# Kernel tuning notes

Hardware: AMD Instinct MI355X
Metric: run time of the kernel (lower is better)

Reference implementation:

```python
import jax, jax.numpy as jnp
import numpy as np

N = 50000      # nodes
E = 800000     # edges (before self loops)
IN_DIM = 128
HID = 16
HEADS = 8
OUT_DIM = 40
NEG_SLOPE = 0.2


def setup_inputs() -> dict:
    key = jax.random.key(0)
    ks = jax.random.split(key, 10)
    x = jax.random.normal(ks[0], (N, IN_DIM), jnp.float32)
    edge_index = jax.random.randint(ks[1], (2, E), 0, N, dtype=jnp.int32)
    # layer 1: GATConv(IN_DIM, HID, heads=HEADS, concat=True)
    W1 = jax.random.normal(ks[2], (IN_DIM, HEADS * HID), jnp.float32) / np.sqrt(IN_DIM).astype(np.float32)
    att_src1 = jax.random.normal(ks[3], (HEADS, HID), jnp.float32) * 0.1
    att_dst1 = jax.random.normal(ks[4], (HEADS, HID), jnp.float32) * 0.1
    bias1 = jnp.zeros((HEADS * HID,), jnp.float32)
    # layer 2: GATConv(HEADS*HID, OUT_DIM, heads=1, concat=False)
    W2 = jax.random.normal(ks[5], (HEADS * HID, OUT_DIM), jnp.float32) / np.sqrt(HEADS * HID).astype(np.float32)
    att_src2 = jax.random.normal(ks[6], (1, OUT_DIM), jnp.float32) * 0.1
    att_dst2 = jax.random.normal(ks[7], (1, OUT_DIM), jnp.float32) * 0.1
    bias2 = jnp.zeros((OUT_DIM,), jnp.float32)
    return {"x": x, "W1": W1, "att_src1": att_src1, "att_dst1": att_dst1, "bias1": bias1,
            "W2": W2, "att_src2": att_src2, "att_dst2": att_dst2, "bias2": bias2,
            "edge_index": edge_index}


def gat_conv(x, src, dst, W, att_src, att_dst, bias, heads, dim, concat, num_nodes):
    # h: [N, H, D]
    h = (x @ W).reshape(num_nodes, heads, dim)
    a_src = jnp.sum(h * att_src, axis=-1)  # [N, H]
    a_dst = jnp.sum(h * att_dst, axis=-1)  # [N, H]
    e = a_src[src] + a_dst[dst]            # [E', H]
    e = jnp.where(e > 0, e, NEG_SLOPE * e)  # leaky_relu
    # segment softmax over edges sharing the same target node
    m = jax.ops.segment_max(e, dst, num_segments=num_nodes)  # [N, H]
    e = jnp.exp(e - m[dst])
    s = jax.ops.segment_sum(e, dst, num_segments=num_nodes)  # [N, H]
    alpha = e / (s[dst] + 1e-16)            # [E', H]
    msg = h[src] * alpha[:, :, None]        # [E', H, D]
    out = jax.ops.segment_sum(msg, dst, num_segments=num_nodes)  # [N, H, D]
    if concat:
        out = out.reshape(num_nodes, heads * dim)
    else:
        out = out.mean(axis=1)
    return out + bias


def reference(x, W1, att_src1, att_dst1, bias1, W2, att_src2, att_dst2, bias2, edge_index):
    # add self loops (PyG GATConv default)
    loop = jnp.arange(N, dtype=edge_index.dtype)
    src = jnp.concatenate([edge_index[0], loop])
    dst = jnp.concatenate([edge_index[1], loop])
    # eval mode: dropout (p=0.6) is identity
    h = gat_conv(x, src, dst, W1, att_src1, att_dst1, bias1, HEADS, HID, True, N)
    h = jax.nn.elu(h)
    out = gat_conv(h, src, dst, W2, att_src2, att_dst2, bias2, 1, OUT_DIM, False, N)
    return jax.nn.log_softmax(out, axis=1)
```

## Files before the change

### kernel.cpp

```cpp
#include <hip/hip_runtime.h>
#include <math.h>

#define IN_DIM 128
#define HEADS 8
#define HID 16
#define OUT_DIM 40
#define NEG 0.2f
#define NSLICE 8

typedef short bf16x8 __attribute__((ext_vector_type(8)));
typedef float f32x4 __attribute__((ext_vector_type(4)));

__device__ __forceinline__ unsigned short f32_to_bf16_rne(float v) {
  unsigned u = __float_as_uint(v);
  return (unsigned short)((u + 0x7FFFu + ((u >> 16) & 1u)) >> 16);
}


__global__ void hist_k(const int* __restrict__ ei, int E0, int N, int snode,
                       int* __restrict__ deg) {
  int b = blockIdx.x;
  int slice = b & (NSLICE - 1);
  int e = (b >> 3) * 256 + threadIdx.x;
  int EP = E0 + N;
  if (e >= EP) return;
  int d = (e < E0) ? ei[E0 + e] : (e - E0);
  if (d / snode == slice) atomicAdd(&deg[d], 1);
}

__global__ __launch_bounds__(1024) void scanA_k(const int* __restrict__ deg, int* __restrict__ rp,
                                                int* __restrict__ bsum, int n) {
  __shared__ int wsum[16];
  int tid = threadIdx.x;
  int i = blockIdx.x * 1024 + tid;
  int lane = tid & 63, w = tid >> 6;
  int v = (i < n) ? deg[i] : 0;
  int x = v;
  #pragma unroll
  for (int off = 1; off < 64; off <<= 1) {
    int y = __shfl_up(x, off);
    if (lane >= off) x += y;
  }
  if (lane == 63) wsum[w] = x;
  __syncthreads();
  if (tid < 16) {
    int s = wsum[tid];
    #pragma unroll
    for (int off = 1; off < 16; off <<= 1) {
      int y = __shfl_up(s, off);
      if (tid >= off) s += y;
    }
    wsum[tid] = s;
  }
  __syncthreads();
  int woff = (w == 0) ? 0 : wsum[w - 1];
  if (i < n) rp[i] = woff + x - v;
  if (tid == 0) bsum[blockIdx.x] = wsum[15];
}

__global__ __launch_bounds__(1024) void scanB_k(int* __restrict__ bsum, int nb,
                                                int* __restrict__ rp, int n) {
  __shared__ int wsum[16];
  int tid = threadIdx.x;
  int lane = tid & 63, w = tid >> 6;
  int v = (tid < nb) ? bsum[tid] : 0;
  int x = v;
  #pragma unroll
  for (int off = 1; off < 64; off <<= 1) {
    int y = __shfl_up(x, off);
    if (lane >= off) x += y;
  }
  if (lane == 63) wsum[w] = x;
  __syncthreads();
  if (tid < 16) {
    int s = wsum[tid];
    #pragma unroll
    for (int off = 1; off < 16; off <<= 1) {
      int y = __shfl_up(s, off);
      if (tid >= off) s += y;
    }
    wsum[tid] = s;
  }
  __syncthreads();
  int woff = (w == 0) ? 0 : wsum[w - 1];
  if (tid < nb) bsum[tid] = woff + x - v;
  if (tid == 0) rp[n] = wsum[15];
}

__global__ __launch_bounds__(1024) void scanC_k(int* __restrict__ rp, const int* __restrict__ bsum,
                                                int* __restrict__ cnt, int n) {
  int i = blockIdx.x * 1024 + threadIdx.x;
  if (i < n) {
    int v = rp[i] + bsum[blockIdx.x];
    rp[i] = v;
    cnt[i] = v;
  }
}

__global__ void scatter_k(const int* __restrict__ ei, int E0, int N, int snode,
                          int* __restrict__ cnt, int* __restrict__ csr_src) {
  int b = blockIdx.x;
  int slice = b & (NSLICE - 1);
  int e = (b >> 3) * 256 + threadIdx.x;
  int EP = E0 + N;
  if (e >= EP) return;
  int d = (e < E0) ? ei[E0 + e] : (e - E0);
  if (d / snode != slice) return;
  int s = (e < E0) ? ei[e] : d;
  int pos = atomicAdd(&cnt[d], 1);
  csr_src[pos] = s;
}

__global__ void prep_k(const float* __restrict__ W1, const float* __restrict__ as1,
                       const float* __restrict__ ad1, const float* __restrict__ W2,
                       const float* __restrict__ as2, const float* __restrict__ ad2,
                       unsigned short* __restrict__ whi, unsigned short* __restrict__ wlo,
                       unsigned short* __restrict__ w2p, int* __restrict__ deg, int N) {
  int t = blockIdx.x * 256 + threadIdx.x;
  if (t < N) deg[t] = 0;
  if (t < 18432) {
    int j = t & 7, lane = (t >> 3) & 63, kc = (t >> 9) & 3, ct = t >> 11;
    int k = kc * 32 + (lane >> 4) * 8 + j;
    int col = lane & 15;
    float v;
    if (ct < 8) {
      v = W1[k * 128 + ct * 16 + col];
    } else {
      int h = col & 7;
      const float* att = (col < 8) ? as1 : ad1;
      float s = 0.f;
      #pragma unroll
      for (int d = 0; d < 16; ++d) s += W1[k * 128 + h * 16 + d] * att[h * 16 + d];
      v = s;
    }
    unsigned u = __float_as_uint(v);
    unsigned hi = (u + 0x7FFFu + ((u >> 16) & 1u)) >> 16;
    float rem = v - __uint_as_float(hi << 16);
    unsigned ur = __float_as_uint(rem);
    unsigned lo = (ur + 0x7FFFu + ((ur >> 16) & 1u)) >> 16;
    whi[t] = (unsigned short)hi;
    wlo[t] = (unsigned short)lo;
  } else if (t < 18432 + 6144) {
    int u2 = t - 18432;
    int j = u2 & 7, lane = (u2 >> 3) & 63, kc = (u2 >> 9) & 3, ct = u2 >> 11;
    int k = kc * 32 + (lane >> 4) * 8 + j;
    int col = ct * 16 + (lane & 15);
    float v;
    if (col < OUT_DIM) {
      v = W2[k * OUT_DIM + col];
    } else if (col < 42) {
      const float* att = (col == OUT_DIM) ? as2 : ad2;
      float s = 0.f;
      #pragma unroll 8
      for (int d = 0; d < OUT_DIM; ++d) s += W2[k * OUT_DIM + d] * att[d];
      v = s;
    } else {
      v = 0.f;
    }
    w2p[u2] = f32_to_bf16_rne(v);
  }
}

__global__ __launch_bounds__(256) void gemm1_mfma_k(
    const float* __restrict__ x, const unsigned short* __restrict__ whi,
    const unsigned short* __restrict__ wlo,
    unsigned short* __restrict__ h1, float* __restrict__ a1s, float* __restrict__ a1d, int N) {
  int w = threadIdx.x >> 6, lane = threadIdx.x & 63;
  int quad = lane >> 4, l15 = lane & 15;
  int row = blockIdx.x * 64 + w * 16 + l15;
  int rowc = (row < N) ? row : (N - 1);

  f32x4 acc[9];
  #pragma unroll
  for (int t = 0; t < 9; ++t) acc[t] = (f32x4){0.f, 0.f, 0.f, 0.f};

  const float* xr = x + (size_t)rowc * 128 + quad * 8;
  #pragma unroll
  for (int kc = 0; kc < 4; ++kc) {
    f32x4 a0 = *reinterpret_cast<const f32x4*>(xr + kc * 32);
    f32x4 a1 = *reinterpret_cast<const f32x4*>(xr + kc * 32 + 4);
    float av[8] = {a0.x, a0.y, a0.z, a0.w, a1.x, a1.y, a1.z, a1.w};
    bf16x8 ahi, alo;
    #pragma unroll
    for (int j = 0; j < 8; ++j) {
      unsigned u = __float_as_uint(av[j]);
      unsigned hi = (u + 0x7FFFu + ((u >> 16) & 1u)) >> 16;
      float rem = av[j] - __uint_as_float(hi << 16);
      unsigned ur = __float_as_uint(rem);
      unsigned lo = (ur + 0x7FFFu + ((ur >> 16) & 1u)) >> 16;
      ahi[j] = (short)hi;
      alo[j] = (short)lo;
    }
    #pragma unroll
    for (int ct = 0; ct < 9; ++ct) {
      bf16x8 bh = *reinterpret_cast<const bf16x8*>(whi + ((size_t)(ct * 4 + kc) * 64 + lane) * 8);
      bf16x8 bl = *reinterpret_cast<const bf16x8*>(wlo + ((size_t)(ct * 4 + kc) * 64 + lane) * 8);
      acc[ct] = __builtin_amdgcn_mfma_f32_16x16x32_bf16(ahi, bh, acc[ct], 0, 0, 0);
      acc[ct] = __builtin_amdgcn_mfma_f32_16x16x32_bf16(ahi, bl, acc[ct], 0, 0, 0);
      acc[ct] = __builtin_amdgcn_mfma_f32_16x16x32_bf16(alo, bh, acc[ct], 0, 0, 0);
    }
  }
  int rbase = blockIdx.x * 64 + w * 16 + quad * 4;
  #pragma unroll
  for (int reg = 0; reg < 4; ++reg) {
    int r = rbase + reg;
    if (r < N) {
      #pragma unroll
      for (int ct = 0; ct < 8; ++ct)
        h1[(size_t)r * 128 + ct * 16 + l15] = f32_to_bf16_rne(acc[ct][reg]);
      float v = acc[8][reg];
      if (l15 < 8) a1s[r * 8 + l15] = v;
      else         a1d[r * 8 + (l15 - 8)] = v;
    }
  }
}

__global__ __launch_bounds__(256) void agg1_k(
    const int* __restrict__ row_ptr, const int* __restrict__ csr_src,
    const float* __restrict__ a1s, const float* __restrict__ a1d,
    const unsigned* __restrict__ h1u, const float* __restrict__ bias1,
    unsigned* __restrict__ vrowp, int N) {
  int wid = threadIdx.x >> 6;
  int lane = threadIdx.x & 63;
  int n = blockIdx.x * 4 + wid;

  __shared__ __align__(16) float wls_s[4][8 * 132];
  __shared__ __align__(16) int   srcs_s[4][128];

  if (n >= N) return;
  float* wls  = wls_s[wid];
  int*   srcs = srcs_s[wid];

  int rs = row_ptr[n], re = row_ptr[n + 1];
  int deg = re - rs;
  int slot = lane >> 3, hw = lane & 7;
  float adn = a1d[n * 8 + hw];

  float sw = 0.f;
  for (int i0 = 0; i0 < deg; i0 += 8) {
    int idx = i0 + slot;
    bool val = idx < deg;
    int s = csr_src[rs + (val ? idx : deg - 1)];
    float e = a1s[s * 8 + hw] + adn;
    e = fmaxf(e, NEG * e);
    float w = val ? __expf(e) : 0.f;
    sw += w;
    if (val && idx < 128) {
      wls[hw * 132 + idx] = w;
      if (hw == 0) srcs[idx] = s;
    }
  }
  sw += __shfl_xor(sw, 8);
  sw += __shfl_xor(sw, 16);
  sw += __shfl_xor(sw, 32);
  int h = lane >> 3;
  float inv = __shfl(1.f / (sw + 1e-16f), h);

  float accx = 0.f, accy = 0.f;
  int lim = (deg < 128) ? deg : 128;
  const float* wh = wls + h * 132;
  int i = 0;
  for (; i + 8 <= lim; i += 8) {
    int4 sa = *reinterpret_cast<const int4*>(srcs + i);
    int4 sb = *reinterpret_cast<const int4*>(srcs + i + 4);
    float4 wa = *reinterpret_cast<const float4*>(wh + i);
    float4 wb = *reinterpret_cast<const float4*>(wh + i + 4);
    unsigned u0 = h1u[(size_t)sa.x * 64 + lane];
    unsigned u1 = h1u[(size_t)sa.y * 64 + lane];
    unsigned u2 = h1u[(size_t)sa.z * 64 + lane];
    unsigned u3 = h1u[(size_t)sa.w * 64 + lane];
    unsigned u4 = h1u[(size_t)sb.x * 64 + lane];
    unsigned u5 = h1u[(size_t)sb.y * 64 + lane];
    unsigned u6 = h1u[(size_t)sb.z * 64 + lane];
    unsigned u7 = h1u[(size_t)sb.w * 64 + lane];
    accx += wa.x * __uint_as_float(u0 << 16) + wa.y * __uint_as_float(u1 << 16)
          + wa.z * __uint_as_float(u2 << 16) + wa.w * __uint_as_float(u3 << 16)
          + wb.x * __uint_as_float(u4 << 16) + wb.y * __uint_as_float(u5 << 16)
          + wb.z * __uint_as_float(u6 << 16) + wb.w * __uint_as_float(u7 << 16);
    accy += wa.x * __uint_as_float(u0 & 0xFFFF0000u) + wa.y * __uint_as_float(u1 & 0xFFFF0000u)
          + wa.z * __uint_as_float(u2 & 0xFFFF0000u) + wa.w * __uint_as_float(u3 & 0xFFFF0000u)
          + wb.x * __uint_as_float(u4 & 0xFFFF0000u) + wb.y * __uint_as_float(u5 & 0xFFFF0000u)
          + wb.z * __uint_as_float(u6 & 0xFFFF0000u) + wb.w * __uint_as_float(u7 & 0xFFFF0000u);
  }
  for (; i < lim; ++i) {
    int s = srcs[i];
    float w = wh[i];
    unsigned u = h1u[(size_t)s * 64 + lane];
    accx += w * __uint_as_float(u << 16);
    accy += w * __uint_as_float(u & 0xFFFF0000u);
  }
  if (deg > 128) {
    float adn2 = a1d[n * 8 + h];
    for (int j2 = 128; j2 < deg; ++j2) {
      int s = csr_src[rs + j2];
      float e = a1s[s * 8 + h] + adn2;
      e = fmaxf(e, NEG * e);
      float w = __expf(e);
      unsigned u = h1u[(size_t)s * 64 + lane];
      accx += w * __uint_as_float(u << 16);
      accy += w * __uint_as_float(u & 0xFFFF0000u);
    }
  }
  float2 b = *reinterpret_cast<const float2*>(bias1 + 2 * lane);
  float vx = accx * inv + b.x;
  float vy = accy * inv + b.y;
  vx = (vx > 0.f) ? vx : (__expf(vx) - 1.f);
  vy = (vy > 0.f) ? vy : (__expf(vy) - 1.f);
  unsigned packed = (unsigned)f32_to_bf16_rne(vx) | ((unsigned)f32_to_bf16_rne(vy) << 16);
  vrowp[(size_t)n * 64 + lane] = packed;
}

__global__ __launch_bounds__(256) void gemm2_mfma_k(
    const unsigned short* __restrict__ vrow, const unsigned short* __restrict__ w2p,
    unsigned short* __restrict__ h2, float* __restrict__ a2s, float* __restrict__ a2d, int N) {
  int w = threadIdx.x >> 6, lane = threadIdx.x & 63;
  int quad = lane >> 4, l15 = lane & 15;
  int row = blockIdx.x * 64 + w * 16 + l15;
  int rowc = (row < N) ? row : (N - 1);

  f32x4 acc[3];
  #pragma unroll
  for (int t = 0; t < 3; ++t) acc[t] = (f32x4){0.f, 0.f, 0.f, 0.f};

  const unsigned short* vr = vrow + (size_t)rowc * 128 + quad * 8;
  #pragma unroll
  for (int kc = 0; kc < 4; ++kc) {
    bf16x8 a = *reinterpret_cast<const bf16x8*>(vr + kc * 32);
    #pragma unroll
    for (int ct = 0; ct < 3; ++ct) {
      bf16x8 bfrag = *reinterpret_cast<const bf16x8*>(w2p + ((size_t)(ct * 4 + kc) * 64 + lane) * 8);
      acc[ct] = __builtin_amdgcn_mfma_f32_16x16x32_bf16(a, bfrag, acc[ct], 0, 0, 0);
    }
  }
  int rbase = blockIdx.x * 64 + w * 16 + quad * 4;
  #pragma unroll
  for (int reg = 0; reg < 4; ++reg) {
    int r = rbase + reg;
    if (r < N) {
      #pragma unroll
      for (int ct = 0; ct < 3; ++ct) {
        int col = ct * 16 + l15;
        float v = acc[ct][reg];
        if (col < OUT_DIM)       h2[(size_t)r * 64 + col] = f32_to_bf16_rne(v);
        else if (col == OUT_DIM) a2s[r] = v;
        else if (col == 41)      a2d[r] = v;
      }
    }
  }
}

__global__ __launch_bounds__(256) void agg2_k(
    const int* __restrict__ row_ptr, const int* __restrict__ csr_src,
    const float* __restrict__ a2s, const float* __restrict__ a2d,
    const unsigned short* __restrict__ h2, const float* __restrict__ bias2,
    float* __restrict__ out, int N) {
  int wid = threadIdx.x >> 6;
  int lane = threadIdx.x & 63;
  int n = blockIdx.x * 4 + wid;

  __shared__ __align__(16) float wls_s[4][128];
  __shared__ __align__(16) int   srcs_s[4][128];

  if (n >= N) return;
  float* wls  = wls_s[wid];
  int*   srcs = srcs_s[wid];

  int rs = row_ptr[n], re = row_ptr[n + 1];
  int deg = re - rs;
  float adn = a2d[n];

  float sw = 0.f;
  for (int i0 = 0; i0 < deg; i0 += 64) {
    int idx = i0 + lane;
    bool val = idx < deg;
    int s = csr_src[rs + (val ? idx : deg - 1)];
    float e = a2s[s] + adn;
    e = fmaxf(e, NEG * e);
    float w = val ? __expf(e) : 0.f;
    sw += w;
    if (val && idx < 128) { wls[idx] = w; srcs[idx] = s; }
  }
  #pragma unroll
  for (int off = 32; off > 0; off >>= 1) sw += __shfl_xor(sw, off);
  float inv = 1.f / (sw + 1e-16f);

  bool act = lane < OUT_DIM;
  float acc = 0.f;
  int lim = (deg < 128) ? deg : 128;
  int i = 0;
  for (; i + 8 <= lim; i += 8) {
    int4 sa = *reinterpret_cast<const int4*>(srcs + i);
    int4 sb = *reinterpret_cast<const int4*>(srcs + i + 4);
    float4 wa = *reinterpret_cast<const float4*>(wls + i);
    float4 wb = *reinterpret_cast<const float4*>(wls + i + 4);
    unsigned g0 = h2[(size_t)sa.x * 64 + lane];
    unsigned g1 = h2[(size_t)sa.y * 64 + lane];
    unsigned g2 = h2[(size_t)sa.z * 64 + lane];
    unsigned g3 = h2[(size_t)sa.w * 64 + lane];
    unsigned g4 = h2[(size_t)sb.x * 64 + lane];
    unsigned g5 = h2[(size_t)sb.y * 64 + lane];
    unsigned g6 = h2[(size_t)sb.z * 64 + lane];
    unsigned g7 = h2[(size_t)sb.w * 64 + lane];
    acc += wa.x * __uint_as_float(g0 << 16) + wa.y * __uint_as_float(g1 << 16)
         + wa.z * __uint_as_float(g2 << 16) + wa.w * __uint_as_float(g3 << 16)
         + wb.x * __uint_as_float(g4 << 16) + wb.y * __uint_as_float(g5 << 16)
         + wb.z * __uint_as_float(g6 << 16) + wb.w * __uint_as_float(g7 << 16);
  }
  for (; i < lim; ++i) {
    int s = srcs[i];
    float w = wls[i];
    unsigned g = h2[(size_t)s * 64 + lane];
    acc += w * __uint_as_float(g << 16);
  }
  if (deg > 128) {
    for (int j2 = 128; j2 < deg; ++j2) {
      int s = csr_src[rs + j2];
      float e = a2s[s] + adn;
      e = fmaxf(e, NEG * e);
      float w = __expf(e);
      unsigned g = h2[(size_t)s * 64 + lane];
      acc += w * __uint_as_float(g << 16);
    }
  }
  float v = act ? (acc * inv + bias2[lane]) : -1e30f;
  float vm = v;
  #pragma unroll
  for (int off = 32; off > 0; off >>= 1) vm = fmaxf(vm, __shfl_xor(vm, off));
  float ex = act ? __expf(v - vm) : 0.f;
  float es = ex;
  #pragma unroll
  for (int off = 32; off > 0; off >>= 1) es += __shfl_xor(es, off);
  if (act) out[(size_t)n * OUT_DIM + lane] = v - vm - __logf(es);
}


extern "C" void kernel_launch(void* const* d_in, const int* in_sizes, int n_in,
                              void* d_out, int out_size, void* d_ws, size_t ws_size,
                              hipStream_t stream) {
  const float* x   = (const float*)d_in[0];
  const float* W1  = (const float*)d_in[1];
  const float* as1 = (const float*)d_in[2];
  const float* ad1 = (const float*)d_in[3];
  const float* b1  = (const float*)d_in[4];
  const float* W2  = (const float*)d_in[5];
  const float* as2 = (const float*)d_in[6];
  const float* ad2 = (const float*)d_in[7];
  const float* b2  = (const float*)d_in[8];
  const int*   ei  = (const int*)d_in[9];
  int N  = in_sizes[0] / IN_DIM;
  int E0 = in_sizes[9] / 2;
  int EP = E0 + N;
  int snode = (N + NSLICE - 1) / NSLICE;
  float* out = (float*)d_out;

  char* ws = (char*)d_ws;
  size_t off = 0;
  auto alloc = [&](size_t bytes) {
    char* p = ws + off;
    off += (bytes + 255) & ~size_t(255);
    return p;
  };
  unsigned short* h1   = (unsigned short*)alloc((size_t)N * 128 * 2);
  float* a1s  = (float*)alloc((size_t)N * 8 * 4);
  float* a1d  = (float*)alloc((size_t)N * 8 * 4);
  unsigned*       vrow = (unsigned*)alloc((size_t)N * 64 * 4);
  unsigned short* h2   = (unsigned short*)alloc((size_t)N * 64 * 2);
  float* a2s  = (float*)alloc((size_t)N * 4);
  float* a2d  = (float*)alloc((size_t)N * 4);
  int*   deg  = (int*)alloc((size_t)N * 4);
  int*   cnt  = (int*)alloc((size_t)N * 4);
  int*   rp   = (int*)alloc((size_t)(N + 4) * 4);
  int*   bsum = (int*)alloc((size_t)1024 * 4);
  int*   csr  = (int*)alloc((size_t)EP * 4);
  unsigned short* whi = (unsigned short*)alloc((size_t)18432 * 2);
  unsigned short* wlo = (unsigned short*)alloc((size_t)18432 * 2);
  unsigned short* w2p = (unsigned short*)alloc((size_t)6144 * 2);

  int nb = (N + 1023) / 1024;
  int nchunk = (EP + 255) / 256;
  prep_k<<<(N + 255) / 256, 256, 0, stream>>>(W1, as1, ad1, W2, as2, ad2, whi, wlo, w2p, deg, N);
  hist_k<<<nchunk * NSLICE, 256, 0, stream>>>(ei, E0, N, snode, deg);
  scanA_k<<<nb, 1024, 0, stream>>>(deg, rp, bsum, N);
  scanB_k<<<1, 1024, 0, stream>>>(bsum, nb, rp, N);
  scanC_k<<<nb, 1024, 0, stream>>>(rp, bsum, cnt, N);
  scatter_k<<<nchunk * NSLICE, 256, 0, stream>>>(ei, E0, N, snode, cnt, csr);
  gemm1_mfma_k<<<(N + 63) / 64, 256, 0, stream>>>(x, whi, wlo, h1, a1s, a1d, N);
  agg1_k<<<(N + 3) / 4, 256, 0, stream>>>(rp, csr, a1s, a1d, (const unsigned*)h1, b1, vrow, N);
  gemm2_mfma_k<<<(N + 63) / 64, 256, 0, stream>>>((const unsigned short*)vrow, w2p, h2, a2s, a2d, N);
  agg2_k<<<(N + 3) / 4, 256, 0, stream>>>(rp, csr, a2s, a2d, h2, b2, out, N);
}
```

Before: 270.0 us.

## Fuse degree histogram into GEMM1 launch and restructure aggregation loops

Merges the degree-histogram kernel into the first GEMM launch using extra blocks, so the two independent stages share one grid and one launch. In both aggregation kernels it stages the neighbor indices once into shared memory, processes two edge slots per lane when computing attention weights, and unrolls the gather loop to 16 neighbors for more loads in flight. High-degree nodes (over 128) now take a separate single-pass path that fuses weight computation, sum and accumulation. Costs are higher register pressure from the wider unroll and a GEMM kernel that now carries unrelated histogram blocks.

```diff
diff --git a/kernel.cpp b/kernel.cpp
--- a/kernel.cpp
+++ b/kernel.cpp
@@ -16,17 +16,6 @@
   return (unsigned short)((u + 0x7FFFu + ((u >> 16) & 1u)) >> 16);
 }
 
-
-__global__ void hist_k(const int* __restrict__ ei, int E0, int N, int snode,
-                       int* __restrict__ deg) {
-  int b = blockIdx.x;
-  int slice = b & (NSLICE - 1);
-  int e = (b >> 3) * 256 + threadIdx.x;
-  int EP = E0 + N;
-  if (e >= EP) return;
-  int d = (e < E0) ? ei[E0 + e] : (e - E0);
-  if (d / snode == slice) atomicAdd(&deg[d], 1);
-}
 
 __global__ __launch_bounds__(1024) void scanA_k(const int* __restrict__ deg, int* __restrict__ rp,
                                                 int* __restrict__ bsum, int n) {
@@ -161,10 +150,22 @@
   }
 }
 
-__global__ __launch_bounds__(256) void gemm1_mfma_k(
+__global__ __launch_bounds__(256) void gemm1_hist_k(
     const float* __restrict__ x, const unsigned short* __restrict__ whi,
     const unsigned short* __restrict__ wlo,
-    unsigned short* __restrict__ h1, float* __restrict__ a1s, float* __restrict__ a1d, int N) {
+    unsigned short* __restrict__ h1, float* __restrict__ a1s, float* __restrict__ a1d,
+    int N, int G1,
+    const int* __restrict__ ei, int E0, int snode, int* __restrict__ deg) {
+  if ((int)blockIdx.x >= G1) {
+    int b = blockIdx.x - G1;
+    int slice = b & (NSLICE - 1);
+    int e = (b >> 3) * 256 + threadIdx.x;
+    int EP = E0 + N;
+    if (e >= EP) return;
+    int d = (e < E0) ? ei[E0 + e] : (e - E0);
+    if (d / snode == slice) atomicAdd(&deg[d], 1);
+    return;
+  }
   int w = threadIdx.x >> 6, lane = threadIdx.x & 63;
   int quad = lane >> 4, l15 = lane & 15;
   int row = blockIdx.x * 64 + w * 16 + l15;
@@ -233,74 +234,114 @@
 
   int rs = row_ptr[n], re = row_ptr[n + 1];
   int deg = re - rs;
-  int slot = lane >> 3, hw = lane & 7;
-  float adn = a1d[n * 8 + hw];
-
-  float sw = 0.f;
-  for (int i0 = 0; i0 < deg; i0 += 8) {
-    int idx = i0 + slot;
-    bool val = idx < deg;
-    int s = csr_src[rs + (val ? idx : deg - 1)];
-    float e = a1s[s * 8 + hw] + adn;
-    e = fmaxf(e, NEG * e);
-    float w = val ? __expf(e) : 0.f;
-    sw += w;
-    if (val && idx < 128) {
-      wls[hw * 132 + idx] = w;
-      if (hw == 0) srcs[idx] = s;
-    }
-  }
-  sw += __shfl_xor(sw, 8);
-  sw += __shfl_xor(sw, 16);
-  sw += __shfl_xor(sw, 32);
   int h = lane >> 3;
-  float inv = __shfl(1.f / (sw + 1e-16f), h);
-
-  float accx = 0.f, accy = 0.f;
-  int lim = (deg < 128) ? deg : 128;
-  const float* wh = wls + h * 132;
-  int i = 0;
-  for (; i + 8 <= lim; i += 8) {
-    int4 sa = *reinterpret_cast<const int4*>(srcs + i);
-    int4 sb = *reinterpret_cast<const int4*>(srcs + i + 4);
-    float4 wa = *reinterpret_cast<const float4*>(wh + i);
-    float4 wb = *reinterpret_cast<const float4*>(wh + i + 4);
-    unsigned u0 = h1u[(size_t)sa.x * 64 + lane];
-    unsigned u1 = h1u[(size_t)sa.y * 64 + lane];
-    unsigned u2 = h1u[(size_t)sa.z * 64 + lane];
-    unsigned u3 = h1u[(size_t)sa.w * 64 + lane];
-    unsigned u4 = h1u[(size_t)sb.x * 64 + lane];
-    unsigned u5 = h1u[(size_t)sb.y * 64 + lane];
-    unsigned u6 = h1u[(size_t)sb.z * 64 + lane];
-    unsigned u7 = h1u[(size_t)sb.w * 64 + lane];
-    accx += wa.x * __uint_as_float(u0 << 16) + wa.y * __uint_as_float(u1 << 16)
-          + wa.z * __uint_as_float(u2 << 16) + wa.w * __uint_as_float(u3 << 16)
-          + wb.x * __uint_as_float(u4 << 16) + wb.y * __uint_as_float(u5 << 16)
-          + wb.z * __uint_as_float(u6 << 16) + wb.w * __uint_as_float(u7 << 16);
-    accy += wa.x * __uint_as_float(u0 & 0xFFFF0000u) + wa.y * __uint_as_float(u1 & 0xFFFF0000u)
-          + wa.z * __uint_as_float(u2 & 0xFFFF0000u) + wa.w * __uint_as_float(u3 & 0xFFFF0000u)
-          + wb.x * __uint_as_float(u4 & 0xFFFF0000u) + wb.y * __uint_as_float(u5 & 0xFFFF0000u)
-          + wb.z * __uint_as_float(u6 & 0xFFFF0000u) + wb.w * __uint_as_float(u7 & 0xFFFF0000u);
-  }
-  for (; i < lim; ++i) {
-    int s = srcs[i];
-    float w = wh[i];
-    unsigned u = h1u[(size_t)s * 64 + lane];
-    accx += w * __uint_as_float(u << 16);
-    accy += w * __uint_as_float(u & 0xFFFF0000u);
-  }
-  if (deg > 128) {
-    float adn2 = a1d[n * 8 + h];
-    for (int j2 = 128; j2 < deg; ++j2) {
-      int s = csr_src[rs + j2];
-      float e = a1s[s * 8 + h] + adn2;
+
+  float accx = 0.f, accy = 0.f, inv;
+
+  if (deg <= 128) {
+    for (int i0 = lane; i0 < deg; i0 += 64) srcs[i0] = csr_src[rs + i0];
+    int slot = lane >> 3, hw = lane & 7;
+    float adn = a1d[n * 8 + hw];
+    float sw = 0.f;
+    for (int i0 = 0; i0 < deg; i0 += 16) {
+      int ia = i0 + slot, ib = i0 + 8 + slot;
+      bool va = ia < deg, vb = ib < deg;
+      int sa = srcs[va ? ia : 0];
+      int sb = srcs[vb ? ib : 0];
+      float ea = a1s[sa * 8 + hw] + adn;
+      float eb = a1s[sb * 8 + hw] + adn;
+      ea = fmaxf(ea, NEG * ea);
+      eb = fmaxf(eb, NEG * eb);
+      float wa = va ? __expf(ea) : 0.f;
+      float wb = vb ? __expf(eb) : 0.f;
+      sw += wa + wb;
+      if (va) wls[hw * 132 + ia] = wa;
+      if (vb) wls[hw * 132 + ib] = wb;
+    }
+    sw += __shfl_xor(sw, 8);
+    sw += __shfl_xor(sw, 16);
+    sw += __shfl_xor(sw, 32);
+    inv = __shfl(1.f / (sw + 1e-16f), h);
+
+    const float* wh = wls + h * 132;
+    int i = 0;
+    for (; i + 16 <= deg; i += 16) {
+      int4 sa = *reinterpret_cast<const int4*>(srcs + i);
+      int4 sb = *reinterpret_cast<const int4*>(srcs + i + 4);
+      int4 sc = *reinterpret_cast<const int4*>(srcs + i + 8);
+      int4 sd = *reinterpret_cast<const int4*>(srcs + i + 12);
+      float4 wa = *reinterpret_cast<const float4*>(wh + i);
+      float4 wb = *reinterpret_cast<const float4*>(wh + i + 4);
+      float4 wc = *reinterpret_cast<const float4*>(wh + i + 8);
+      float4 wd = *reinterpret_cast<const float4*>(wh + i + 12);
+      unsigned u0 = h1u[(size_t)sa.x * 64 + lane];
+      unsigned u1 = h1u[(size_t)sa.y * 64 + lane];
+      unsigned u2 = h1u[(size_t)sa.z * 64 + lane];
+      unsigned u3 = h1u[(size_t)sa.w * 64 + lane];
+      unsigned u4 = h1u[(size_t)sb.x * 64 + lane];
+      unsigned u5 = h1u[(size_t)sb.y * 64 + lane];
+      unsigned u6 = h1u[(size_t)sb.z * 64 + lane];
+      unsigned u7 = h1u[(size_t)sb.w * 64 + lane];
+      unsigned u8 = h1u[(size_t)sc.x * 64 + lane];
+      unsigned u9 = h1u[(size_t)sc.y * 64 + lane];
+      unsigned uA = h1u[(size_t)sc.z * 64 + lane];
+      unsigned uB = h1u[(size_t)sc.w * 64 + lane];
+      unsigned uC = h1u[(size_t)sd.x * 64 + lane];
+      unsigned uD = h1u[(size_t)sd.y * 64 + lane];
+      unsigned uE = h1u[(size_t)sd.z * 64 + lane];
+      unsigned uF = h1u[(size_t)sd.w * 64 + lane];
+      accx += wa.x * __uint_as_float(u0 << 16) + wa.y * __uint_as_float(u1 << 16)
+            + wa.z * __uint_as_float(u2 << 16) + wa.w * __uint_as_float(u3 << 16)
+            + wb.x * __uint_as_float(u4 << 16) + wb.y * __uint_as_float(u5 << 16)
+            + wb.z * __uint_as_float(u6 << 16) + wb.w * __uint_as_float(u7 << 16)
+            + wc.x * __uint_as_float(u8 << 16) + wc.y * __uint_as_float(u9 << 16)
+            + wc.z * __uint_as_float(uA << 16) + wc.w * __uint_as_float(uB << 16)
+            + wd.x * __uint_as_float(uC << 16) + wd.y * __uint_as_float(uD << 16)
+            + wd.z * __uint_as_float(uE << 16) + wd.w * __uint_as_float(uF << 16);
+      accy += wa.x * __uint_as_float(u0 & 0xFFFF0000u) + wa.y * __uint_as_float(u1 & 0xFFFF0000u)
+            + wa.z * __uint_as_float(u2 & 0xFFFF0000u) + wa.w * __uint_as_float(u3 & 0xFFFF0000u)
+            + wb.x * __uint_as_float(u4 & 0xFFFF0000u) + wb.y * __uint_as_float(u5 & 0xFFFF0000u)
+            + wb.z * __uint_as_float(u6 & 0xFFFF0000u) + wb.w * __uint_as_float(u7 & 0xFFFF0000u)
+            + wc.x * __uint_as_float(u8 & 0xFFFF0000u) + wc.y * __uint_as_float(u9 & 0xFFFF0000u)
+            + wc.z * __uint_as_float(uA & 0xFFFF0000u) + wc.w * __uint_as_float(uB & 0xFFFF0000u)
+            + wd.x * __uint_as_float(uC & 0xFFFF0000u) + wd.y * __uint_as_float(uD & 0xFFFF0000u)
+            + wd.z * __uint_as_float(uE & 0xFFFF0000u) + wd.w * __uint_as_float(uF & 0xFFFF0000u);
+    }
+    for (; i + 4 <= deg; i += 4) {
+      int4 sa = *reinterpret_cast<const int4*>(srcs + i);
+      float4 wa = *reinterpret_cast<const float4*>(wh + i);
+      unsigned u0 = h1u[(size_t)sa.x * 64 + lane];
+      unsigned u1 = h1u[(size_t)sa.y * 64 + lane];
+      unsigned u2 = h1u[(size_t)sa.z * 64 + lane];
+      unsigned u3 = h1u[(size_t)sa.w * 64 + lane];
+      accx += wa.x * __uint_as_float(u0 << 16) + wa.y * __uint_as_float(u1 << 16)
+            + wa.z * __uint_as_float(u2 << 16) + wa.w * __uint_as_float(u3 << 16);
+      accy += wa.x * __uint_as_float(u0 & 0xFFFF0000u) + wa.y * __uint_as_float(u1 & 0xFFFF0000u)
+            + wa.z * __uint_as_float(u2 & 0xFFFF0000u) + wa.w * __uint_as_float(u3 & 0xFFFF0000u);
+    }
+    for (; i < deg; ++i) {
+      int s = srcs[i];
+      float w = wh[i];
+      unsigned u = h1u[(size_t)s * 64 + lane];
+      accx += w * __uint_as_float(u << 16);
+      accy += w * __uint_as_float(u & 0xFFFF0000u);
+    }
+  } else {
+    float adn = a1d[n * 8 + h];
+    float sw = 0.f;
+    for (int i = rs; i < re; ++i) {
+      int s = csr_src[i];
+      float e = a1s[s * 8 + h] + adn;
       e = fmaxf(e, NEG * e);
       float w = __expf(e);
       unsigned u = h1u[(size_t)s * 64 + lane];
+      sw += w;
       accx += w * __uint_as_float(u << 16);
       accy += w * __uint_as_float(u & 0xFFFF0000u);
     }
-  }
+    inv = 1.f / (sw + 1e-16f);
+  }
+
   float2 b = *reinterpret_cast<const float2*>(bias1 + 2 * lane);
   float vx = accx * inv + b.x;
   float vy = accy * inv + b.y;
@@ -368,60 +409,93 @@
   int rs = row_ptr[n], re = row_ptr[n + 1];
   int deg = re - rs;
   float adn = a2d[n];
-
-  float sw = 0.f;
-  for (int i0 = 0; i0 < deg; i0 += 64) {
-    int idx = i0 + lane;
-    bool val = idx < deg;
-    int s = csr_src[rs + (val ? idx : deg - 1)];
-    float e = a2s[s] + adn;
-    e = fmaxf(e, NEG * e);
-    float w = val ? __expf(e) : 0.f;
-    sw += w;
-    if (val && idx < 128) { wls[idx] = w; srcs[idx] = s; }
-  }
-  #pragma unroll
-  for (int off = 32; off > 0; off >>= 1) sw += __shfl_xor(sw, off);
-  float inv = 1.f / (sw + 1e-16f);
-
   bool act = lane < OUT_DIM;
-  float acc = 0.f;
-  int lim = (deg < 128) ? deg : 128;
-  int i = 0;
-  for (; i + 8 <= lim; i += 8) {
-    int4 sa = *reinterpret_cast<const int4*>(srcs + i);
-    int4 sb = *reinterpret_cast<const int4*>(srcs + i + 4);
-    float4 wa = *reinterpret_cast<const float4*>(wls + i);
-    float4 wb = *reinterpret_cast<const float4*>(wls + i + 4);
-    unsigned g0 = h2[(size_t)sa.x * 64 + lane];
-    unsigned g1 = h2[(size_t)sa.y * 64 + lane];
-    unsigned g2 = h2[(size_t)sa.z * 64 + lane];
-    unsigned g3 = h2[(size_t)sa.w * 64 + lane];
-    unsigned g4 = h2[(size_t)sb.x * 64 + lane];
-    unsigned g5 = h2[(size_t)sb.y * 64 + lane];
-    unsigned g6 = h2[(size_t)sb.z * 64 + lane];
-    unsigned g7 = h2[(size_t)sb.w * 64 + lane];
-    acc += wa.x * __uint_as_float(g0 << 16) + wa.y * __uint_as_float(g1 << 16)
-         + wa.z * __uint_as_float(g2 << 16) + wa.w * __uint_as_float(g3 << 16)
-         + wb.x * __uint_as_float(g4 << 16) + wb.y * __uint_as_float(g5 << 16)
-         + wb.z * __uint_as_float(g6 << 16) + wb.w * __uint_as_float(g7 << 16);
-  }
-  for (; i < lim; ++i) {
-    int s = srcs[i];
-    float w = wls[i];
-    unsigned g = h2[(size_t)s * 64 + lane];
-    acc += w * __uint_as_float(g << 16);
-  }
-  if (deg > 128) {
-    for (int j2 = 128; j2 < deg; ++j2) {
-      int s = csr_src[rs + j2];
+  float acc = 0.f, inv;
+
+  if (deg <= 128) {
+    for (int i0 = lane; i0 < deg; i0 += 64) srcs[i0] = csr_src[rs + i0];
+    int ia = lane, ib = lane + 64;
+    bool va = ia < deg, vb = ib < deg;
+    int sa = srcs[va ? ia : 0];
+    int sb = srcs[vb ? ib : 0];
+    float ea = a2s[sa] + adn;
+    float eb = a2s[sb] + adn;
+    ea = fmaxf(ea, NEG * ea);
+    eb = fmaxf(eb, NEG * eb);
+    float wa = va ? __expf(ea) : 0.f;
+    float wb = vb ? __expf(eb) : 0.f;
+    float sw = wa + wb;
+    if (va) wls[ia] = wa;
+    if (vb) wls[ib] = wb;
+    #pragma unroll
+    for (int off = 32; off > 0; off >>= 1) sw += __shfl_xor(sw, off);
+    inv = 1.f / (sw + 1e-16f);
+
+    int i = 0;
+    for (; i + 16 <= deg; i += 16) {
+      int4 s0 = *reinterpret_cast<const int4*>(srcs + i);
+      int4 s1 = *reinterpret_cast<const int4*>(srcs + i + 4);
+      int4 s2 = *reinterpret_cast<const int4*>(srcs + i + 8);
+      int4 s3 = *reinterpret_cast<const int4*>(srcs + i + 12);
+      float4 w0 = *reinterpret_cast<const float4*>(wls + i);
+      float4 w1 = *reinterpret_cast<const float4*>(wls + i + 4);
+      float4 w2 = *reinterpret_cast<const float4*>(wls + i + 8);
+      float4 w3 = *reinterpret_cast<const float4*>(wls + i + 12);
+      unsigned g0 = h2[(size_t)s0.x * 64 + lane];
+      unsigned g1 = h2[(size_t)s0.y * 64 + lane];
+      unsigned g2 = h2[(size_t)s0.z * 64 + lane];
+      unsigned g3 = h2[(size_t)s0.w * 64 + lane];
+      unsigned g4 = h2[(size_t)s1.x * 64 + lane];
+      unsigned g5 = h2[(size_t)s1.y * 64 + lane];
+      unsigned g6 = h2[(size_t)s1.z * 64 + lane];
+      unsigned g7 = h2[(size_t)s1.w * 64 + lane];
+      unsigned g8 = h2[(size_t)s2.x * 64 + lane];
+      unsigned g9 = h2[(size_t)s2.y * 64 + lane];
+      unsigned gA = h2[(size_t)s2.z * 64 + lane];
+      unsigned gB = h2[(size_t)s2.w * 64 + lane];
+      unsigned gC = h2[(size_t)s3.x * 64 + lane];
+      unsigned gD = h2[(size_t)s3.y * 64 + lane];
+      unsigned gE = h2[(size_t)s3.z * 64 + lane];
+      unsigned gF = h2[(size_t)s3.w * 64 + lane];
+      acc += w0.x * __uint_as_float(g0 << 16) + w0.y * __uint_as_float(g1 << 16)
+           + w0.z * __uint_as_float(g2 << 16) + w0.w * __uint_as_float(g3 << 16)
+           + w1.x * __uint_as_float(g4 << 16) + w1.y * __uint_as_float(g5 << 16)
+           + w1.z * __uint_as_float(g6 << 16) + w1.w * __uint_as_float(g7 << 16)
+           + w2.x * __uint_as_float(g8 << 16) + w2.y * __uint_as_float(g9 << 16)
+           + w2.z * __uint_as_float(gA << 16) + w2.w * __uint_as_float(gB << 16)
+           + w3.x * __uint_as_float(gC << 16) + w3.y * __uint_as_float(gD << 16)
+           + w3.z * __uint_as_float(gE << 16) + w3.w * __uint_as_float(gF << 16);
+    }
+    for (; i + 4 <= deg; i += 4) {
+      int4 s0 = *reinterpret_cast<const int4*>(srcs + i);
+      float4 w0 = *reinterpret_cast<const float4*>(wls + i);
+      unsigned g0 = h2[(size_t)s0.x * 64 + lane];
+      unsigned g1 = h2[(size_t)s0.y * 64 + lane];
+      unsigned g2 = h2[(size_t)s0.z * 64 + lane];
+      unsigned g3 = h2[(size_t)s0.w * 64 + lane];
+      acc += w0.x * __uint_as_float(g0 << 16) + w0.y * __uint_as_float(g1 << 16)
+           + w0.z * __uint_as_float(g2 << 16) + w0.w * __uint_as_float(g3 << 16);
+    }
+    for (; i < deg; ++i) {
+      int s = srcs[i];
+      float w = wls[i];
+      unsigned g = h2[(size_t)s * 64 + lane];
+      acc += w * __uint_as_float(g << 16);
+    }
+  } else {
+    float sw = 0.f;
+    for (int i = rs; i < re; ++i) {
+      int s = csr_src[i];
       float e = a2s[s] + adn;
       e = fmaxf(e, NEG * e);
       float w = __expf(e);
+      sw += w;
       unsigned g = h2[(size_t)s * 64 + lane];
       acc += w * __uint_as_float(g << 16);
     }
-  }
+    inv = 1.f / (sw + 1e-16f);
+  }
+
   float v = act ? (acc * inv + bias2[lane]) : -1e30f;
   float vm = v;
   #pragma unroll
@@ -478,13 +552,14 @@
 
   int nb = (N + 1023) / 1024;
   int nchunk = (EP + 255) / 256;
+  int G1 = (N + 63) / 64;
   prep_k<<<(N + 255) / 256, 256, 0, stream>>>(W1, as1, ad1, W2, as2, ad2, whi, wlo, w2p, deg, N);
-  hist_k<<<nchunk * NSLICE, 256, 0, stream>>>(ei, E0, N, snode, deg);
+  gemm1_hist_k<<<G1 + nchunk * NSLICE, 256, 0, stream>>>(x, whi, wlo, h1, a1s, a1d, N, G1,
+                                                         ei, E0, snode, deg);
   scanA_k<<<nb, 1024, 0, stream>>>(deg, rp, bsum, N);
   scanB_k<<<1, 1024, 0, stream>>>(bsum, nb, rp, N);
   scanC_k<<<nb, 1024, 0, stream>>>(rp, bsum, cnt, N);
   scatter_k<<<nchunk * NSLICE, 256, 0, stream>>>(ei, E0, N, snode, cnt, csr);
-  gemm1_mfma_k<<<(N + 63) / 64, 256, 0, stream>>>(x, whi, wlo, h1, a1s, a1d, N);
   agg1_k<<<(N + 3) / 4, 256, 0, stream>>>(rp, csr, a1s, a1d, (const unsigned*)h1, b1, vrow, N);
   gemm2_mfma_k<<<(N + 63) / 64, 256, 0, stream>>>((const unsigned short*)vrow, w2p, h2, a2s, a2d, N);
   agg2_k<<<(N + 3) / 4, 256, 0, stream>>>(rp, csr, a2s, a2d, h2, b2, out, N);
```

Measured after the change: 258.0 us. -4.5%, faster.
